# Optimization experiments

Measured on AMD Instinct MI355X. Metric: run time of the kernel, lower is better.

## Reference

```python
import jax, jax.numpy as jnp
import numpy as np

B, N, D, H = 2, 2048, 1024, 16
HD = D // H  # head_dim = 64
LN_EPS = 1e-5


def rotate_half(x):
    # x: [..., HD] with interleaved pairs -> (-x2, x1) interleaved back
    x = x.reshape(*x.shape[:-1], HD // 2, 2)
    x1, x2 = x[..., 0], x[..., 1]
    return jnp.stack((-x2, x1), axis=-1).reshape(*x.shape[:-2], HD)


def setup_inputs() -> dict:
    key = jax.random.key(0)
    ks = jax.random.split(key, 12)
    s = 0.02
    return {
        "descriptor": jax.random.normal(ks[0], (B, N, D), dtype=jnp.float32),
        "encoding": jax.random.normal(ks[1], (2, B, H, N, HD), dtype=jnp.float32),
        "w_qkv": s * jax.random.normal(ks[2], (3 * D, D), dtype=jnp.float32),
        "b_qkv": jnp.zeros((3 * D,), dtype=jnp.float32),
        "w_out": s * jax.random.normal(ks[3], (D, D), dtype=jnp.float32),
        "b_out": jnp.zeros((D,), dtype=jnp.float32),
        "w_ffn1": s * jax.random.normal(ks[4], (2 * D, 2 * D), dtype=jnp.float32),
        "b_ffn1": jnp.zeros((2 * D,), dtype=jnp.float32),
        "ln_g": jnp.ones((2 * D,), dtype=jnp.float32),
        "ln_b": jnp.zeros((2 * D,), dtype=jnp.float32),
        "w_ffn2": s * jax.random.normal(ks[5], (D, 2 * D), dtype=jnp.float32),
        "b_ffn2": jnp.zeros((D,), dtype=jnp.float32),
    }


def reference(descriptor, encoding, w_qkv, b_qkv, w_out, b_out,
              w_ffn1, b_ffn1, ln_g, ln_b, w_ffn2, b_ffn2):
    # fused QKV projection; last dim laid out as (H, HD, 3) like the torch code
    qkv = descriptor @ w_qkv.T + b_qkv                      # [B, N, 3D]
    qkv = qkv.reshape(B, N, H, HD, 3).transpose(0, 2, 1, 3, 4)  # [B, H, N, HD, 3]
    q, k, v = qkv[..., 0], qkv[..., 1], qkv[..., 2]

    # cached rotary embedding
    q = q * encoding[0] + rotate_half(q) * encoding[1]
    k = k * encoding[0] + rotate_half(k) * encoding[1]

    # scaled dot-product attention (no mask)
    scale = 1.0 / jnp.sqrt(jnp.asarray(HD, dtype=q.dtype))
    scores = jnp.einsum('bhqd,bhkd->bhqk', q, k) * scale    # [B, H, N, N]
    attn = jax.nn.softmax(scores, axis=-1)
    context = jnp.einsum('bhqk,bhkd->bhqd', attn, v)        # [B, H, N, HD]

    message = context.transpose(0, 2, 1, 3).reshape(B, N, D) @ w_out.T + b_out

    # concat-FFN: Linear -> LayerNorm -> GELU -> Linear
    h = jnp.concatenate([descriptor, message], axis=-1) @ w_ffn1.T + b_ffn1  # [B, N, 2D]
    mu = jnp.mean(h, axis=-1, keepdims=True)
    var = jnp.mean(jnp.square(h - mu), axis=-1, keepdims=True)
    h = (h - mu) * jax.lax.rsqrt(var + LN_EPS) * ln_g + ln_b
    h = jax.nn.gelu(h, approximate=False)
    return descriptor + h @ w_ffn2.T + b_ffn2
```

## Files before the change

### kernel.cpp

```cpp
#include <hip/hip_runtime.h>
#include <hip/hip_bf16.h>
#include <stdint.h>
#include <stddef.h>

#define B_   2
#define N_   2048
#define D_   1024
#define H_   16
#define HD_  64
#define BH_  (B_ * H_)
#define M_   (B_ * N_)

typedef short bf16x8 __attribute__((ext_vector_type(8)));
typedef float f32x4  __attribute__((ext_vector_type(4)));

static __device__ __forceinline__ unsigned short f2bf(float f) {
    union { float f; unsigned u; } c; c.f = f;
    unsigned r = (c.u + 0x7FFFu + ((c.u >> 16) & 1u)) >> 16;
    return (unsigned short)r;
}
static __device__ __forceinline__ float bf2f(unsigned short u) {
    union { unsigned u; float f; } c; c.u = ((unsigned)u) << 16; return c.f;
}

#define GLDS16(g, l)                                                                     \
    __builtin_amdgcn_global_load_lds((const __attribute__((address_space(1))) void*)(g), \
                                     (__attribute__((address_space(3))) void*)(l), 16, 0, 0)

#define QSCALE 0.18033688011112042f

__global__ __launch_bounds__(256) void k_cast_w4(const float* __restrict__ s0,
                                                 const float* __restrict__ s1,
                                                 const float* __restrict__ s2,
                                                 const float* __restrict__ s3,
                                                 unsigned short* __restrict__ d0,
                                                 unsigned short* __restrict__ d1,
                                                 unsigned short* __restrict__ d2,
                                                 unsigned short* __restrict__ d3) {
    int i = blockIdx.x * 256 + threadIdx.x;
    const float* s; unsigned short* d; int off;
    if (i < 786432)              { s = s0; d = d0; off = i; }
    else if (i < 1048576)        { s = s1; d = d1; off = i - 786432; }
    else if (i < 2097152)        { s = s2; d = d2; off = i - 1048576; }
    else                         { s = s3; d = d3; off = i - 2097152; }
    float4 v = *(const float4*)(s + (size_t)off * 4);
    ushort4 o;
    o.x = f2bf(v.x); o.y = f2bf(v.y); o.z = f2bf(v.z); o.w = f2bf(v.w);
    *(ushort4*)(d + (size_t)off * 4) = o;
}

__global__ __launch_bounds__(256) void k_cast_desc(const float* __restrict__ in,
                                                   unsigned short* __restrict__ cat) {
    int i = (blockIdx.x * 256 + threadIdx.x) * 4;
    float4 v = *(const float4*)(in + i);
    int row = i >> 10, col = i & 1023;
    ushort4 o;
    o.x = f2bf(v.x); o.y = f2bf(v.y); o.z = f2bf(v.z); o.w = f2bf(v.w);
    *(ushort4*)(cat + (size_t)row * 2048 + col) = o;
}

template <int EPI>
__global__ __launch_bounds__(256) void k_gemm(const unsigned short* __restrict__ A, int lda,
                                              const unsigned short* __restrict__ Bm, int ldb,
                                              void* __restrict__ Cv, int ldc,
                                              const float* __restrict__ bias,
                                              const float* __restrict__ resid, int ldr,
                                              unsigned short* __restrict__ qd,
                                              unsigned short* __restrict__ kd,
                                              unsigned short* __restrict__ vd,
                                              int K) {
    __shared__ unsigned short As[128 * 64];
    __shared__ unsigned short Bs[128 * 64];
    const int tid  = threadIdx.x;
    const int wave = tid >> 6, lane = tid & 63;
    const int wr = wave >> 1, wc = wave & 1;
    const int brow = blockIdx.y * 128, bcol = blockIdx.x * 128;

    const int srow = (lane >> 3);
    const int scol = (lane & 7) * 8;
    const int frow = lane & 15;
    const int fk   = (lane >> 4) * 8;

    f32x4 acc[4][4] = {};

    for (int kt = 0; kt < K; kt += 64) {
        __syncthreads();
#pragma unroll
        for (int j = 0; j < 4; ++j) {
            int r = wave * 32 + j * 8 + srow;
            GLDS16(A  + (size_t)(brow + r) * lda + kt + scol, (char*)As + wave * 4096 + j * 1024);
            GLDS16(Bm + (size_t)(bcol + r) * ldb + kt + scol, (char*)Bs + wave * 4096 + j * 1024);
        }
        __syncthreads();
#pragma unroll
        for (int ks = 0; ks < 2; ++ks) {
            bf16x8 a[4], b[4];
#pragma unroll
            for (int m = 0; m < 4; ++m)
                a[m] = *(const bf16x8*)(As + (wr * 64 + m * 16 + frow) * 64 + ks * 32 + fk);
#pragma unroll
            for (int n = 0; n < 4; ++n)
                b[n] = *(const bf16x8*)(Bs + (wc * 64 + n * 16 + frow) * 64 + ks * 32 + fk);
#pragma unroll
            for (int m = 0; m < 4; ++m)
#pragma unroll
                for (int n = 0; n < 4; ++n)
                    acc[m][n] = __builtin_amdgcn_mfma_f32_16x16x32_bf16(a[m], b[n], acc[m][n], 0, 0, 0);
        }
    }

    const int orow = (lane >> 4) * 4;
#pragma unroll
    for (int m = 0; m < 4; ++m) {
        int row0 = brow + wr * 64 + m * 16 + orow;
#pragma unroll
        for (int n = 0; n < 4; ++n) {
            int col = bcol + wc * 64 + n * 16 + frow;
            float bs = bias[col];
#pragma unroll
            for (int r = 0; r < 4; ++r) {
                float v = acc[m][n][r] + bs;
                if (EPI == 3) {
                    int row = row0 + r;
                    int bb = row >> 11, nr = row & (N_ - 1);
                    int h = col / 192;
                    int rem = col - h * 192;
                    int d = rem / 3;
                    int c = rem - d * 3;
                    unsigned short* dst = (c == 0) ? qd : (c == 1) ? kd : vd;
                    dst[(((size_t)(bb * H_ + h)) * N_ + nr) * 64 + d] = f2bf(v);
                } else if (EPI == 2) {
                    v += resid[(size_t)(row0 + r) * ldr + col];
                    ((float*)Cv)[(size_t)(row0 + r) * ldc + col] = v;
                } else {
                    ((unsigned short*)Cv)[(size_t)(row0 + r) * ldc + col] = f2bf(v);
                }
            }
        }
    }
}

__global__ __launch_bounds__(256) void k_rope_ip(unsigned short* __restrict__ Qb,
                                                 unsigned short* __restrict__ Kb,
                                                 const float* __restrict__ enc) {
    int idx = blockIdx.x * 256 + threadIdx.x;
    int i  = idx & 31;
    int n  = (idx >> 5) & (N_ - 1);
    int bh = idx >> 16;
    size_t eoff = ((size_t)bh * N_ + n) * 64 + i * 2;
    float2 e0 = *(const float2*)(enc + eoff);
    float2 e1 = *(const float2*)(enc + (size_t)BH_ * N_ * 64 + eoff);
    ushort2 qp = *(const ushort2*)(Qb + eoff);
    ushort2 kp = *(const ushort2*)(Kb + eoff);
    float q1 = bf2f(qp.x), q2 = bf2f(qp.y);
    float k1 = bf2f(kp.x), k2 = bf2f(kp.y);
    ushort2 qo, ko;
    qo.x = f2bf((q1 * e0.x - q2 * e1.x) * QSCALE);
    qo.y = f2bf((q2 * e0.y + q1 * e1.y) * QSCALE);
    ko.x = f2bf(k1 * e0.x - k2 * e1.x);
    ko.y = f2bf(k2 * e0.y + k1 * e1.y);
    *(ushort2*)(Qb + eoff) = qo;
    *(ushort2*)(Kb + eoff) = ko;
}

__global__ __launch_bounds__(256) void k_transpose_v(const unsigned short* __restrict__ Vb,
                                                     unsigned short* __restrict__ Vt) {
    __shared__ unsigned short t[64][72];
    int bh = blockIdx.y, n0 = blockIdx.x * 64;
    int tid = threadIdx.x;
    int r  = tid >> 2;
    int c0 = (tid & 3) * 16;
    const unsigned short* src = Vb + ((size_t)bh * N_ + n0 + r) * 64 + c0;
    *(bf16x8*)(&t[r][c0])     = *(const bf16x8*)(src);
    *(bf16x8*)(&t[r][c0 + 8]) = *(const bf16x8*)(src + 8);
    __syncthreads();
    int d  = tid >> 2;
    int nc = (tid & 3) * 16;
    bf16x8 o0, o1;
#pragma unroll
    for (int j = 0; j < 8; ++j) { o0[j] = (short)t[nc + j][d]; o1[j] = (short)t[nc + 8 + j][d]; }
    unsigned short* dst = Vt + ((size_t)bh * 64 + d) * N_ + n0 + nc;
    *(bf16x8*)(dst)     = o0;
    *(bf16x8*)(dst + 8) = o1;
}

__global__ __launch_bounds__(256) void k_attn(const unsigned short* __restrict__ Qb,
                                              const unsigned short* __restrict__ Kb,
                                              const unsigned short* __restrict__ Vt,
                                              unsigned short* __restrict__ Ctx) {
    __shared__ unsigned short Ks[2][64 * 64];
    __shared__ unsigned short Vs[2][64 * 64];
    __shared__ unsigned short Ps[4][16 * 64];

    int lin = blockIdx.x + 32 * blockIdx.y;
    int ixc = lin >> 3;
    int bh  = (lin & 7) * 4 + (ixc >> 5);
    int q0  = (ixc & 31) * 64;
    int b = bh >> 4, h = bh & 15;
    int tid = threadIdx.x, wave = tid >> 6, lane = tid & 63;
    int frow = lane & 15, fk = (lane >> 4) * 8, g = lane >> 4;
    int f7x8 = (frow & 7) * 8;

    int srow = lane >> 3;
    int scol = ((lane & 7) ^ srow) * 8;

    const unsigned short* Kbh = Kb + (size_t)bh * N_ * 64;
    const unsigned short* Vbh = Vt + (size_t)bh * 64 * N_;

#define ATTN_STAGE(bufi, kt)                                                           \
    do {                                                                               \
        _Pragma("unroll")                                                              \
        for (int j = 0; j < 2; ++j) {                                                  \
            int rr = wave * 16 + j * 8 + srow;                                         \
            GLDS16(Kbh + (size_t)((kt) + rr) * 64 + scol,                              \
                   (char*)Ks[bufi] + wave * 2048 + j * 1024);                          \
            GLDS16(Vbh + (size_t)rr * N_ + (kt) + scol,                                \
                   (char*)Vs[bufi] + wave * 2048 + j * 1024);                          \
        }                                                                              \
    } while (0)

    const unsigned short* qptr = Qb + ((size_t)bh * N_ + q0 + wave * 16 + frow) * 64;
    bf16x8 qf[2];
    qf[0] = *(const bf16x8*)(qptr + fk);
    qf[1] = *(const bf16x8*)(qptr + 32 + fk);

    float mrow[4] = {-INFINITY, -INFINITY, -INFINITY, -INFINITY};
    float lrow[4] = {0.f, 0.f, 0.f, 0.f};
    f32x4 accO[4] = {};

    ATTN_STAGE(0, 0);

    for (int t = 0; t < N_ / 64; ++t) {
        int cur = t & 1;
        __syncthreads();
        if (t + 1 < N_ / 64) ATTN_STAGE(cur ^ 1, (t + 1) * 64);

        f32x4 s[4];
        __builtin_amdgcn_s_setprio(1);
#pragma unroll
        for (int kc = 0; kc < 4; ++kc) {
            f32x4 a = {};
#pragma unroll
            for (int ks = 0; ks < 2; ++ks) {
                bf16x8 kfr = *(const bf16x8*)(Ks[cur] + (kc * 16 + frow) * 64 + ((ks * 32 + fk) ^ f7x8));
                a = __builtin_amdgcn_mfma_f32_16x16x32_bf16(qf[ks], kfr, a, 0, 0, 0);
            }
            s[kc] = a;
        }
        __builtin_amdgcn_s_setprio(0);

        float scl[4];
#pragma unroll
        for (int r = 0; r < 4; ++r) {
            float mx = fmaxf(fmaxf(s[0][r], s[1][r]), fmaxf(s[2][r], s[3][r]));
            mx = fmaxf(mx, __shfl_xor(mx, 1));
            mx = fmaxf(mx, __shfl_xor(mx, 2));
            mx = fmaxf(mx, __shfl_xor(mx, 4));
            mx = fmaxf(mx, __shfl_xor(mx, 8));
            float mn = fmaxf(mrow[r], mx);
            float sc = exp2f(mrow[r] - mn);
            mrow[r] = mn;
            float ps = 0.f;
#pragma unroll
            for (int kc = 0; kc < 4; ++kc) {
                float p = exp2f(s[kc][r] - mn);
                s[kc][r] = p;
                ps += p;
            }
            ps += __shfl_xor(ps, 1);
            ps += __shfl_xor(ps, 2);
            ps += __shfl_xor(ps, 4);
            ps += __shfl_xor(ps, 8);
            lrow[r] = lrow[r] * sc + ps;
            scl[r] = sc;
        }
#pragma unroll
        for (int df = 0; df < 4; ++df)
#pragma unroll
            for (int r = 0; r < 4; ++r) accO[df][r] *= scl[r];

#pragma unroll
        for (int kc = 0; kc < 4; ++kc)
#pragma unroll
            for (int r = 0; r < 4; ++r) {
                int prow = g * 4 + r;
                Ps[wave][prow * 64 + ((kc * 16 + frow) ^ ((prow & 7) * 8))] = f2bf(s[kc][r]);
            }
        asm volatile("s_waitcnt lgkmcnt(0)" ::: "memory");
        __builtin_amdgcn_sched_barrier(0);

        __builtin_amdgcn_s_setprio(1);
#pragma unroll
        for (int ks = 0; ks < 2; ++ks) {
            bf16x8 pa = *(const bf16x8*)(&Ps[wave][frow * 64 + ((ks * 32 + fk) ^ f7x8)]);
#pragma unroll
            for (int df = 0; df < 4; ++df) {
                bf16x8 vf = *(const bf16x8*)(Vs[cur] + (df * 16 + frow) * 64 + ((ks * 32 + fk) ^ f7x8));
                accO[df] = __builtin_amdgcn_mfma_f32_16x16x32_bf16(pa, vf, accO[df], 0, 0, 0);
            }
        }
        __builtin_amdgcn_s_setprio(0);
    }

    float inv[4];
#pragma unroll
    for (int r = 0; r < 4; ++r) inv[r] = 1.0f / lrow[r];
#pragma unroll
    for (int df = 0; df < 4; ++df)
#pragma unroll
        for (int r = 0; r < 4; ++r) {
            int q = q0 + wave * 16 + g * 4 + r;
            Ctx[((size_t)(b * N_ + q)) * D_ + h * 64 + df * 16 + frow] = f2bf(accO[df][r] * inv[r]);
        }
#undef ATTN_STAGE
}

__global__ __launch_bounds__(256) void k_ln_gelu(const unsigned short* __restrict__ hsrc,
                                                 const float* __restrict__ gma,
                                                 const float* __restrict__ bta,
                                                 unsigned short* __restrict__ out) {
    __shared__ float red[2][4];
    int row = blockIdx.x, tid = threadIdx.x;
    const unsigned short* hr = hsrc + (size_t)row * 2048 + tid * 8;
    bf16x8 hv = *(const bf16x8*)(hr);
    float xs[8];
    float s = 0.f, q = 0.f;
#pragma unroll
    for (int j = 0; j < 8; ++j) {
        float x = bf2f((unsigned short)hv[j]);
        xs[j] = x; s += x; q += x * x;
    }
#pragma unroll
    for (int off = 1; off < 64; off <<= 1) {
        s += __shfl_xor(s, off);
        q += __shfl_xor(q, off);
    }
    int wave = tid >> 6;
    if ((tid & 63) == 0) { red[0][wave] = s; red[1][wave] = q; }
    __syncthreads();
    s = red[0][0] + red[0][1] + red[0][2] + red[0][3];
    q = red[1][0] + red[1][1] + red[1][2] + red[1][3];
    float mu   = s * (1.f / 2048.f);
    float var  = q * (1.f / 2048.f) - mu * mu;
    float rstd = rsqrtf(var + 1e-5f);
    int c = tid * 8;
#pragma unroll
    for (int j = 0; j < 8; ++j) {
        float x = (xs[j] - mu) * rstd * gma[c + j] + bta[c + j];
        float y = 0.5f * x * (1.f + erff(x * 0.70710678118654752f));
        out[(size_t)row * 2048 + c + j] = f2bf(y);
    }
}

extern "C" void kernel_launch(void* const* d_in, const int* in_sizes, int n_in,
                              void* d_out, int out_size, void* d_ws, size_t ws_size,
                              hipStream_t stream) {
    const float* descriptor = (const float*)d_in[0];
    const float* encoding   = (const float*)d_in[1];
    const float* w_qkv      = (const float*)d_in[2];
    const float* b_qkv      = (const float*)d_in[3];
    const float* w_out      = (const float*)d_in[4];
    const float* b_out      = (const float*)d_in[5];
    const float* w_ffn1     = (const float*)d_in[6];
    const float* b_ffn1     = (const float*)d_in[7];
    const float* ln_g       = (const float*)d_in[8];
    const float* ln_b       = (const float*)d_in[9];
    const float* w_ffn2     = (const float*)d_in[10];
    const float* b_ffn2     = (const float*)d_in[11];
    float* out = (float*)d_out;

    char* ws = (char*)d_ws;
    unsigned short* wffn1_b = (unsigned short*)(ws);
    unsigned short* wffn2_b = (unsigned short*)(ws + ((size_t)8  << 20));
    unsigned short* wout_b  = (unsigned short*)(ws + ((size_t)12 << 20));
    unsigned short* cat     = (unsigned short*)(ws + ((size_t)14 << 20));
    unsigned short* Qb      = (unsigned short*)(ws + ((size_t)30 << 20));
    unsigned short* Kb      = (unsigned short*)(ws + ((size_t)38 << 20));
    unsigned short* Vb      = (unsigned short*)(ws + ((size_t)46 << 20));
    unsigned short* wqkv_b  = (unsigned short*)(ws + ((size_t)54 << 20));
    unsigned short* Vt      = (unsigned short*)(ws + ((size_t)54 << 20));
    unsigned short* msg     = (unsigned short*)(ws + ((size_t)46 << 20));
    unsigned short* hbuf    = (unsigned short*)(ws + ((size_t)30 << 20));
    unsigned short* h2      = (unsigned short*)(ws + ((size_t)14 << 20));

    k_cast_desc<<<4096, 256, 0, stream>>>(descriptor, cat);
    k_cast_w4<<<10240, 256, 0, stream>>>(w_qkv, w_out, w_ffn1, w_ffn2,
                                         wqkv_b, wout_b, wffn1_b, wffn2_b);

    k_gemm<3><<<dim3(24, 32), 256, 0, stream>>>(cat, 2048, wqkv_b, 1024, nullptr, 0,
                                                b_qkv, nullptr, 0, Qb, Kb, Vb, 1024);
    k_rope_ip<<<8192, 256, 0, stream>>>(Qb, Kb, encoding);
    k_transpose_v<<<dim3(32, 32), 256, 0, stream>>>(Vb, Vt);
    k_attn<<<dim3(32, 32), 256, 0, stream>>>(Qb, Kb, Vt, msg);
    k_gemm<1><<<dim3(8, 32), 256, 0, stream>>>(msg, 1024, wout_b, 1024, cat + 1024, 2048,
                                               b_out, nullptr, 0, nullptr, nullptr, nullptr, 1024);
    k_gemm<1><<<dim3(16, 32), 256, 0, stream>>>(cat, 2048, wffn1_b, 2048, hbuf, 2048,
                                                b_ffn1, nullptr, 0, nullptr, nullptr, nullptr, 2048);
    k_ln_gelu<<<4096, 256, 0, stream>>>(hbuf, ln_g, ln_b, h2);
    k_gemm<2><<<dim3(8, 32), 256, 0, stream>>>(h2, 2048, wffn2_b, 2048, out, 1024,
                                               b_ffn2, descriptor, 1024, nullptr, nullptr, nullptr, 2048);
}
```

Baseline: 482.1 us.

## Compute transposed attention scores so softmax row reductions stay lane-local

```diff
diff --git a/kernel.cpp b/kernel.cpp
--- a/kernel.cpp
+++ b/kernel.cpp
@@ -224,8 +224,8 @@
     qf[0] = *(const bf16x8*)(qptr + fk);
     qf[1] = *(const bf16x8*)(qptr + 32 + fk);
 
-    float mrow[4] = {-INFINITY, -INFINITY, -INFINITY, -INFINITY};
-    float lrow[4] = {0.f, 0.f, 0.f, 0.f};
+    float m = -INFINITY;
+    float l = 0.f;
     f32x4 accO[4] = {};
 
     ATTN_STAGE(0, 0);
@@ -235,7 +235,7 @@
         __syncthreads();
         if (t + 1 < N_ / 64) ATTN_STAGE(cur ^ 1, (t + 1) * 64);
 
-        f32x4 s[4];
+        f32x4 st[4];
         __builtin_amdgcn_s_setprio(1);
 #pragma unroll
         for (int kc = 0; kc < 4; ++kc) {
@@ -243,49 +243,52 @@
 #pragma unroll
             for (int ks = 0; ks < 2; ++ks) {
                 bf16x8 kfr = *(const bf16x8*)(Ks[cur] + (kc * 16 + frow) * 64 + ((ks * 32 + fk) ^ f7x8));
-                a = __builtin_amdgcn_mfma_f32_16x16x32_bf16(qf[ks], kfr, a, 0, 0, 0);
+                a = __builtin_amdgcn_mfma_f32_16x16x32_bf16(kfr, qf[ks], a, 0, 0, 0);
             }
-            s[kc] = a;
+            st[kc] = a;
         }
         __builtin_amdgcn_s_setprio(0);
 
-        float scl[4];
-#pragma unroll
-        for (int r = 0; r < 4; ++r) {
-            float mx = fmaxf(fmaxf(s[0][r], s[1][r]), fmaxf(s[2][r], s[3][r]));
-            mx = fmaxf(mx, __shfl_xor(mx, 1));
-            mx = fmaxf(mx, __shfl_xor(mx, 2));
-            mx = fmaxf(mx, __shfl_xor(mx, 4));
-            mx = fmaxf(mx, __shfl_xor(mx, 8));
-            float mn = fmaxf(mrow[r], mx);
-            float sc = exp2f(mrow[r] - mn);
-            mrow[r] = mn;
-            float ps = 0.f;
-#pragma unroll
-            for (int kc = 0; kc < 4; ++kc) {
-                float p = exp2f(s[kc][r] - mn);
-                s[kc][r] = p;
+        float mloc = fmaxf(fmaxf(fmaxf(st[0][0], st[0][1]), fmaxf(st[0][2], st[0][3])),
+                           fmaxf(fmaxf(st[1][0], st[1][1]), fmaxf(st[1][2], st[1][3])));
+        mloc = fmaxf(mloc,
+               fmaxf(fmaxf(fmaxf(st[2][0], st[2][1]), fmaxf(st[2][2], st[2][3])),
+                     fmaxf(fmaxf(st[3][0], st[3][1]), fmaxf(st[3][2], st[3][3]))));
+        mloc = fmaxf(mloc, __shfl_xor(mloc, 16));
+        mloc = fmaxf(mloc, __shfl_xor(mloc, 32));
+        float mn = fmaxf(m, mloc);
+        float sc = exp2f(m - mn);
+        m = mn;
+        float ps = 0.f;
+#pragma unroll
+        for (int kc = 0; kc < 4; ++kc)
+#pragma unroll
+            for (int r = 0; r < 4; ++r) {
+                float p = exp2f(st[kc][r] - mn);
+                st[kc][r] = p;
                 ps += p;
             }
-            ps += __shfl_xor(ps, 1);
-            ps += __shfl_xor(ps, 2);
-            ps += __shfl_xor(ps, 4);
-            ps += __shfl_xor(ps, 8);
-            lrow[r] = lrow[r] * sc + ps;
-            scl[r] = sc;
-        }
+        ps += __shfl_xor(ps, 16);
+        ps += __shfl_xor(ps, 32);
+        l = l * sc + ps;
+
+        float scl[4];
+#pragma unroll
+        for (int r = 0; r < 4; ++r) scl[r] = __shfl(sc, g * 4 + r);
 #pragma unroll
         for (int df = 0; df < 4; ++df)
 #pragma unroll
             for (int r = 0; r < 4; ++r) accO[df][r] *= scl[r];
 
 #pragma unroll
-        for (int kc = 0; kc < 4; ++kc)
-#pragma unroll
-            for (int r = 0; r < 4; ++r) {
-                int prow = g * 4 + r;
-                Ps[wave][prow * 64 + ((kc * 16 + frow) ^ ((prow & 7) * 8))] = f2bf(s[kc][r]);
-            }
+        for (int kc = 0; kc < 4; ++kc) {
+            unsigned lo, hi;
+            asm("v_cvt_pk_bf16_f32 %0, %1, %2" : "=v"(lo) : "v"(st[kc][0]), "v"(st[kc][1]));
+            asm("v_cvt_pk_bf16_f32 %0, %1, %2" : "=v"(hi) : "v"(st[kc][2]), "v"(st[kc][3]));
+            int col = (kc * 16 + g * 4) ^ f7x8;
+            uint2 w; w.x = lo; w.y = hi;
+            *(uint2*)(&Ps[wave][frow * 64 + col]) = w;
+        }
         asm volatile("s_waitcnt lgkmcnt(0)" ::: "memory");
         __builtin_amdgcn_sched_barrier(0);
 
@@ -304,7 +307,7 @@
 
     float inv[4];
 #pragma unroll
-    for (int r = 0; r < 4; ++r) inv[r] = 1.0f / lrow[r];
+    for (int r = 0; r < 4; ++r) inv[r] = 1.0f / __shfl(l, g * 4 + r);
 #pragma unroll
     for (int df = 0; df < 4; ++df)
 #pragma unroll
```

New measurement: 455.1 us. 1.06x faster.
